# Performance work log

Measured on AMD Instinct MI355X. Metric: run time of the kernel, lower is better.

## Reference

```python
import jax, jax.numpy as jnp
import numpy as np

T, H, E, K, I = 8192, 1024, 8, 2, 512  # tokens, hidden, experts, top_k, expert_intermediate
IS = I * 1  # shared-expert intermediate = expert_intermediate_size * num_shared_experts


def setup_inputs() -> dict:
    key = jax.random.key(0)
    ks = jax.random.split(key, 6)
    s = lambda *d: 1.0 / np.sqrt(d[0])
    return {
        "hidden_states": jax.random.normal(ks[0], (T, H), dtype=jnp.float32),
        "w_gate": jax.random.normal(ks[1], (H, E), dtype=jnp.float32) * s(H),
        "w_experts_gate_up": jax.random.normal(ks[2], (E, H, 2 * I), dtype=jnp.float32) * s(H),
        "w_experts_down": jax.random.normal(ks[3], (E, I, H), dtype=jnp.float32) * s(I),
        "w_shared_gate_up": jax.random.normal(ks[4], (H, 2 * IS), dtype=jnp.float32) * s(H),
        "w_shared_down": jax.random.normal(ks[5], (IS, H), dtype=jnp.float32) * s(IS),
    }


def _silu_and_mul(gu):
    d = gu.shape[-1] // 2
    return jax.nn.silu(gu[..., :d]) * gu[..., d:]


def reference(hidden_states, w_gate, w_experts_gate_up, w_experts_down,
              w_shared_gate_up, w_shared_down):
    x = hidden_states  # [T, H]

    # shared expert: SwiGLU MLP (reduce_results=False path)
    shared_out = _silu_and_mul(x @ w_shared_gate_up) @ w_shared_down  # [T, H]

    # router gate + top-k with renormalization (norm_expert_prob=True)
    router_logits = x @ w_gate  # [T, E]
    probs = jax.nn.softmax(router_logits.astype(jnp.float32), axis=-1)
    topk_w, topk_idx = jax.lax.top_k(probs, K)  # [T, K]
    topk_w = topk_w / jnp.sum(topk_w, axis=-1, keepdims=True)
    # scatter top-k weights into a sparse [T, E] combine matrix
    full_w = jnp.zeros((T, E), dtype=x.dtype)
    full_w = full_w.at[jnp.arange(T)[:, None], topk_idx].set(topk_w.astype(x.dtype))

    # expert SwiGLU MLPs (grouped GEMM expressed as batched einsum over experts)
    gu = jnp.einsum('th,ehi->eti', x, w_experts_gate_up)       # [E, T, 2I]
    act = _silu_and_mul(gu)                                     # [E, T, I]
    expert_out = jnp.einsum('eti,eih->eth', act, w_experts_down)  # [E, T, H]

    # weighted combine over selected experts (weights are zero elsewhere)
    moe_out = jnp.einsum('te,eth->th', full_w, expert_out)     # [T, H]

    return moe_out + shared_out
```

## Files before the change

### kernel.cpp

```cpp
#include <hip/hip_runtime.h>
#include <hip/hip_bf16.h>
#include <cstdint>

#define T_TOK 8192
#define HID   1024
#define NE    9
#define ISZ   512
#define RBASE 18432
#define NSLOT (RBASE + T_TOK)

#define BM 256
#define NROWB (NSLOT / BM)

typedef unsigned short u16;
typedef unsigned int   u32;
typedef signed char    i8;
typedef __attribute__((ext_vector_type(8))) short short8;
typedef __attribute__((ext_vector_type(4))) float f32x4;
typedef __attribute__((ext_vector_type(4))) int   i32x4;

__device__ __forceinline__ u16 f2bf(float f) {
  u32 u = __builtin_bit_cast(u32, f);
  return (u16)((u + 0x7fffu + ((u >> 16) & 1u)) >> 16);
}
__device__ __forceinline__ float bf2f(u16 v) {
  return __builtin_bit_cast(float, (u32)v << 16);
}
__device__ __forceinline__ int q8(float v, float inv) {
  int q = (int)__builtin_rintf(v * inv);
  return (q > 127) ? 127 : ((q < -127) ? -127 : q);
}

#define STAGE(gp, lp) __builtin_amdgcn_global_load_lds( \
    (__attribute__((address_space(1))) u32*)(gp),       \
    (__attribute__((address_space(3))) u32*)(lp), 16, 0, 0)

__global__ void k_zero(int* wam) { if (threadIdx.x < 16) wam[threadIdx.x] = 0; }

__global__ __launch_bounds__(256) void k_wamax(
    const float* __restrict__ wgu, const float* __restrict__ wsg, int* __restrict__ wam) {
  const int e = blockIdx.y;
  const float* src = (e < 8) ? (wgu + (size_t)e * 1048576) : wsg;
  float m = 0.f;
  for (int i = blockIdx.x * 256 + threadIdx.x; i < 262144; i += 16 * 256) {
    float4 v = ((const float4*)src)[i];
    m = fmaxf(m, fmaxf(fmaxf(fabsf(v.x), fabsf(v.y)), fmaxf(fabsf(v.z), fabsf(v.w))));
  }
#pragma unroll
  for (int off = 32; off >= 1; off >>= 1) m = fmaxf(m, __shfl_xor(m, off));
  __shared__ float sm[4];
  if ((threadIdx.x & 63) == 0) sm[threadIdx.x >> 6] = m;
  __syncthreads();
  if (threadIdx.x == 0) {
    m = fmaxf(fmaxf(sm[0], sm[1]), fmaxf(sm[2], sm[3]));
    atomicMax(wam + e, __float_as_int(m));
  }
}

#define NB_WGUP (32 * 32 * NE)
#define NB_WDN  (32 * 16 * NE)
#define NB_RTR  (T_TOK / 4)

__global__ __launch_bounds__(256) void k_prep(
    const float* __restrict__ x, const float* __restrict__ wg,
    const float* __restrict__ wgu, const float* __restrict__ wsg,
    const float* __restrict__ wdn, const float* __restrict__ wsd,
    const int* __restrict__ wam,
    i8* __restrict__ xq, float* __restrict__ sxg,
    i8* __restrict__ wguq, u16* __restrict__ wdT,
    int* __restrict__ eidx, float2* __restrict__ wts) {
  __shared__ float tile[32][33];
  const int b = blockIdx.x;
  const int tid = threadIdx.x;

  if (b < NB_WGUP) {
    const int e = b / 1024, rem = b % 1024;
    const int c0 = (rem & 31) * 32, h0 = (rem >> 5) * 32;
    const float* src = (e < 8) ? (wgu + (size_t)e * HID * 1024) : wsg;
    const float invw = 127.f / __int_as_float(wam[e]);
    const int tx = tid & 31, ty = tid >> 5;
    for (int i = ty; i < 32; i += 8)
      tile[i][tx] = src[(size_t)(h0 + i) * 1024 + c0 + tx];
    __syncthreads();
    for (int j = ty; j < 32; j += 8) {
      int c = c0 + j;
      int i = (c < 512) ? c : (c - 512);
      int colp = ((i >> 4) * 32) + ((c < 512) ? 0 : 16) + (i & 15);
      wguq[((size_t)e * 1024 + colp) * HID + h0 + tx] = (i8)q8(tile[tx][j], invw);
    }
    return;
  }
  if (b < NB_WGUP + NB_WDN) {
    const int bb = b - NB_WGUP;
    const int e = bb / 512, rem = bb % 512;
    const int h0 = (rem & 31) * 32, i0 = (rem >> 5) * 32;
    const float* src = (e < 8) ? (wdn + (size_t)e * ISZ * HID) : wsd;
    const int tx = tid & 31, ty = tid >> 5;
    for (int a = ty; a < 32; a += 8)
      tile[a][tx] = src[(size_t)(i0 + a) * HID + h0 + tx];
    __syncthreads();
    for (int j = ty; j < 32; j += 8)
      wdT[((size_t)e * HID + h0 + j) * ISZ + i0 + tx] = f2bf(tile[tx][j]);
    return;
  }
  const int t = (b - NB_WGUP - NB_WDN) * 4 + (tid >> 6);
  const int l = tid & 63;
  float a[8] = {0, 0, 0, 0, 0, 0, 0, 0};
  float vals[16];
  float am = 0.f;
  const float4* xr4 = (const float4*)(x + (size_t)t * HID);
#pragma unroll
  for (int j = 0; j < 4; ++j) {
    const float4 v = xr4[j * 64 + l];
    vals[4 * j] = v.x; vals[4 * j + 1] = v.y; vals[4 * j + 2] = v.z; vals[4 * j + 3] = v.w;
    am = fmaxf(am, fmaxf(fmaxf(fabsf(v.x), fabsf(v.y)), fmaxf(fabsf(v.z), fabsf(v.w))));
    const int h = (j * 64 + l) * 4;
#pragma unroll
    for (int i = 0; i < 4; ++i) {
      const float4 w0 = *(const float4*)&wg[(h + i) * 8];
      const float4 w1 = *(const float4*)&wg[(h + i) * 8 + 4];
      const float ev = vals[4 * j + i];
      a[0] += ev * w0.x; a[1] += ev * w0.y; a[2] += ev * w0.z; a[3] += ev * w0.w;
      a[4] += ev * w1.x; a[5] += ev * w1.y; a[6] += ev * w1.z; a[7] += ev * w1.w;
    }
  }
#pragma unroll
  for (int off = 32; off >= 1; off >>= 1) {
    am = fmaxf(am, __shfl_xor(am, off));
#pragma unroll
    for (int e2 = 0; e2 < 8; ++e2) a[e2] += __shfl_xor(a[e2], off);
  }
  const float inv = (am > 0.f) ? 127.f / am : 0.f;
  u32* xq4 = (u32*)(xq + (size_t)t * HID);
#pragma unroll
  for (int j = 0; j < 4; ++j) {
    u32 q = ((u32)(unsigned char)(i8)q8(vals[4 * j], inv)) |
            ((u32)(unsigned char)(i8)q8(vals[4 * j + 1], inv) << 8) |
            ((u32)(unsigned char)(i8)q8(vals[4 * j + 2], inv) << 16) |
            ((u32)(unsigned char)(i8)q8(vals[4 * j + 3], inv) << 24);
    xq4[j * 64 + l] = q;
  }
  if (l == 0) {
    sxg[t] = am * (1.f / 127.f);
    int ia = 0;
#pragma unroll
    for (int e2 = 1; e2 < 8; ++e2) if (a[e2] > a[ia]) ia = e2;
    int ib = (ia == 0) ? 1 : 0;
#pragma unroll
    for (int e2 = 0; e2 < 8; ++e2) if (e2 != ia && a[e2] > a[ib]) ib = e2;
    float wa = 1.f / (1.f + expf(a[ib] - a[ia]));
    eidx[t] = ia | (ib << 8);
    wts[t] = make_float2(wa, 1.f - wa);
  }
}

__global__ __launch_bounds__(512) void k_scatter(
    const int* __restrict__ eidx, int* __restrict__ btok, int* __restrict__ slotmap,
    int* __restrict__ seg, int* __restrict__ segcnt) {
  __shared__ int cnt_s[8];
  __shared__ int goff_s[9];
  const int e = threadIdx.x >> 6;
  const int l = threadIdx.x & 63;

  int c1 = 0;
  for (int c = 0; c < T_TOK / 64; ++c) {
    int v = eidx[c * 64 + l];
    c1 += __popcll(__ballot((v & 255) == e)) + __popcll(__ballot(((v >> 8) & 255) == e));
  }
  if (l == 0) cnt_s[e] = c1;
  __syncthreads();
  if (threadIdx.x == 0) {
    int off = 0;
    for (int k = 0; k < 8; ++k) { goff_s[k] = off; off += (cnt_s[k] + 255) & ~255; }
    goff_s[8] = off;
  }
  __syncthreads();
  const int base0 = goff_s[e];
  const int cnt_e = cnt_s[e];
  const unsigned long long below = (l == 63) ? ~0ull >> 1 : ((1ull << l) - 1);

  int base = base0;
  for (int c = 0; c < T_TOK / 64; ++c) {
    const int t = c * 64 + l;
    const int v = eidx[t];
    const unsigned long long ma = __ballot((v & 255) == e);
    const unsigned long long mb = __ballot(((v >> 8) & 255) == e);
    if ((v & 255) == e) {
      int s = base + __popcll(ma & below);
      btok[s] = t; slotmap[2 * t] = s;
    }
    if (((v >> 8) & 255) == e) {
      int s = base + __popcll(ma) + __popcll(mb & below);
      btok[s] = t; slotmap[2 * t + 1] = s;
    }
    base += __popcll(ma) + __popcll(mb);
  }
  for (int p = cnt_e + l; p < ((cnt_e + 255) & ~255); p += 64) btok[base0 + p] = 0;
  if (threadIdx.x < 9) seg[threadIdx.x] = goff_s[threadIdx.x];
  if (threadIdx.x < 8) segcnt[threadIdx.x] = cnt_s[threadIdx.x];
}

__device__ __forceinline__ bool seg_lookup(const int* __restrict__ seg,
                                           const int* __restrict__ segcnt,
                                           int brow, int& e) {
  if (brow >= RBASE) { e = 8; return true; }
  if (brow >= seg[8]) return false;
  e = 0;
#pragma unroll
  for (int k = 1; k < 8; ++k) if (brow >= seg[k]) e = k;
  return brow < seg[e] + segcnt[e];
}


#define G1_STG(kt) do {                                             \
    const int _ra = ((kt) % 3) * 32768;                             \
    STAGE(sA0 + (kt) * 128, Ab + _ra + 0 * 8192 + w * 1024);        \
    STAGE(sA1 + (kt) * 128, Ab + _ra + 1 * 8192 + w * 1024);        \
    STAGE(sA2 + (kt) * 128, Ab + _ra + 2 * 8192 + w * 1024);        \
    STAGE(sA3 + (kt) * 128, Ab + _ra + 3 * 8192 + w * 1024);        \
    const int _rb = ((kt) % 3) * 16384;                             \
    STAGE(sB0 + (kt) * 128, Bb + _rb + 0 * 8192 + w * 1024);        \
    STAGE(sB1 + (kt) * 128, Bb + _rb + 1 * 8192 + w * 1024); } while (0)

#define G1_LOADF(SA, SB, RG, KX) do {                               \
    _Pragma("unroll") for (int m = 0; m < 4; ++m)                   \
      SA[m] = *(const i32x4*)&Ab[(RG) * 32768 + aBase + m * 2048 + (KX)]; \
    _Pragma("unroll") for (int n = 0; n < 4; ++n)                   \
      SB[n] = *(const i32x4*)&Bb[(RG) * 16384 + bBase + n * 2048 + (KX)]; } while (0)

#define G1_MFMA(SA, SB) do { __builtin_amdgcn_s_setprio(1);         \
    _Pragma("unroll") for (int m = 0; m < 4; ++m)                   \
      _Pragma("unroll") for (int n = 0; n < 4; ++n)                 \
        acc[m][n] = __builtin_amdgcn_mfma_i32_16x16x64_i8(SA[m], SB[n], acc[m][n], 0, 0, 0); \
    __builtin_amdgcn_s_setprio(0); } while (0)

__global__ __launch_bounds__(512) void k_gemm_gu(
    const i8* __restrict__ xq,
    const i8* __restrict__ wguq,
    const int* __restrict__ seg, const int* __restrict__ segcnt,
    const int* __restrict__ btok, const float* __restrict__ sxg,
    const int* __restrict__ wam,
    u16* __restrict__ act)
{
  const int bid = blockIdx.x;
  const int brow = (bid % NROWB) * BM;
  const int bcol = (bid / NROWB) * 128;
  int e;
  if (!seg_lookup(seg, segcnt, brow, e)) return;

  __shared__ __align__(16) i8 Ab[3 * 32768];
  __shared__ __align__(16) i8 Bb[3 * 16384];
  __shared__ float sxl[BM];

  const int tid = threadIdx.x;
  const int w = tid >> 6, l = tid & 63;
  const int wm = w >> 1, wn = w & 1;
  const int fr = l & 15, fg = l >> 4;

  if (tid < BM) {
    const int rrow = brow + tid;
    const int tk = (e < 8) ? btok[rrow] : (rrow - RBASE);
    sxl[tid] = sxg[tk];
  }

  const int rr = w * 8 + (l >> 3);
  const int sw = ((l & 7) ^ (l >> 3)) * 16;
  int tr[4];
#pragma unroll
  for (int j = 0; j < 4; ++j) {
    const int gr = brow + j * 64 + rr;
    tr[j] = (e < 8) ? btok[gr] : (gr - RBASE);
  }
  const i8* sA0 = xq + (size_t)tr[0] * HID + sw;
  const i8* sA1 = xq + (size_t)tr[1] * HID + sw;
  const i8* sA2 = xq + (size_t)tr[2] * HID + sw;
  const i8* sA3 = xq + (size_t)tr[3] * HID + sw;
  const i8* sB0 = wguq + ((size_t)e * 1024 + bcol + 0 * 64 + rr) * HID + sw;
  const i8* sB1 = wguq + ((size_t)e * 1024 + bcol + 1 * 64 + rr) * HID + sw;

  const int aBase = (wm * 64 + fr) * 128;
  const int bBase = (wn * 64 + fr) * 128;
  const int kx0 = (fg ^ (fr & 7)) * 16;
  const int kx1 = kx0 ^ 64;

  i32x4 acc[4][4];
#pragma unroll
  for (int m = 0; m < 4; ++m)
#pragma unroll
    for (int n = 0; n < 4; ++n) acc[m][n] = (i32x4){0, 0, 0, 0};
  i32x4 fA0[4], fB0[4], fA1[4], fB1[4];

  const int NKT = HID / 128;
  G1_STG(0); G1_STG(1);
  asm volatile("s_waitcnt vmcnt(6)" ::: "memory");
  __builtin_amdgcn_s_barrier();
  for (int s = 0; s < NKT; ++s) {
    const int rg = s % 3;
    if (s + 2 < NKT) G1_STG(s + 2);
    G1_LOADF(fA0, fB0, rg, kx0);
    __builtin_amdgcn_sched_barrier(0);
    G1_LOADF(fA1, fB1, rg, kx1);
    asm volatile("s_waitcnt lgkmcnt(8)" ::: "memory");
    __builtin_amdgcn_sched_barrier(0);
    G1_MFMA(fA0, fB0);
    asm volatile("s_waitcnt lgkmcnt(0)" ::: "memory");
    __builtin_amdgcn_sched_barrier(0);
    G1_MFMA(fA1, fB1);
    if (s + 1 < NKT) {
      if (s + 2 < NKT) { asm volatile("s_waitcnt vmcnt(6)" ::: "memory"); }
      else             { asm volatile("s_waitcnt vmcnt(0)" ::: "memory"); }
      __builtin_amdgcn_s_barrier();
    }
  }

  const float swe = __int_as_float(wam[e]) * (1.f / 127.f);
#pragma unroll
  for (int m = 0; m < 4; ++m) {
#pragma unroll
    for (int p = 0; p < 2; ++p) {
      const i32x4 gI = acc[m][2 * p], uI = acc[m][2 * p + 1];
      const int col = ((bcol + wn * 64) >> 1) + p * 16 + fr;
#pragma unroll
      for (int r = 0; r < 4; ++r) {
        const int row_l = wm * 64 + m * 16 + fg * 4 + r;
        const float sc = sxl[row_l] * swe;
        const float gate = (float)gI[r] * sc;
        const float up   = (float)uI[r] * sc;
        const float sv = gate / (1.f + __expf(-gate));
        act[(size_t)(brow + row_l) * ISZ + col] = f2bf(sv * up);
      }
    }
  }
}


#define D_STGA(kt) do { const int _d = ((kt) % 3) * 8192 + w * 1024; \
    STAGE(dA0 + (kt) * 32, As + _d);                                 \
    STAGE(dA1 + (kt) * 32, As + _d + 512); } while (0)
#define D_STGB(kt) do { const int _d = ((kt) % 3) * 8192 + w * 1024; \
    STAGE(dB0 + (kt) * 32, Bs + _d);                                 \
    STAGE(dB1 + (kt) * 32, Bs + _d + 512); } while (0)
#define D_LDA4(sl, mb) do {                                          \
    af[0] = *(const short8*)&As[(sl) + aOff + ((mb) + 0) * 512];     \
    af[1] = *(const short8*)&As[(sl) + aOff + ((mb) + 1) * 512];     \
    af[2] = *(const short8*)&As[(sl) + aOff + ((mb) + 2) * 512];     \
    af[3] = *(const short8*)&As[(sl) + aOff + ((mb) + 3) * 512]; } while (0)
#define D_LDB4(sl) do {                                              \
    bf[0] = *(const short8*)&Bs[(sl) + bOff + 0 * 512];              \
    bf[1] = *(const short8*)&Bs[(sl) + bOff + 1 * 512];              \
    bf[2] = *(const short8*)&Bs[(sl) + bOff + 2 * 512];              \
    bf[3] = *(const short8*)&Bs[(sl) + bOff + 3 * 512]; } while (0)
#define D_MFMA16(mb) do { __builtin_amdgcn_s_setprio(1);             \
    _Pragma("unroll") for (int mm = 0; mm < 4; ++mm)                 \
      _Pragma("unroll") for (int nn = 0; nn < 4; ++nn)               \
        accf[(mb) + mm][nn] = __builtin_amdgcn_mfma_f32_16x16x32_bf16( \
            af[mm], bf[nn], accf[(mb) + mm][nn], 0, 0, 0);           \
    __builtin_amdgcn_s_setprio(0); } while (0)

__global__ __launch_bounds__(512) void k_gemm_down(
    const u16* __restrict__ act, const u16* __restrict__ wdT,
    const int* __restrict__ seg, const int* __restrict__ segcnt,
    u16* __restrict__ tmp) {
  const int brow = blockIdx.x * BM;
  const int bcol = blockIdx.y * 256;
  int e;
  if (!seg_lookup(seg, segcnt, brow, e)) return;

  __shared__ __align__(16) u16 As[3 * 8192];
  __shared__ __align__(16) u16 Bs[3 * 8192];

  const int tid = threadIdx.x;
  const int w = tid >> 6, l = tid & 63;
  const int wm = w >> 2, wn = w & 3;
  const int fr = l & 15, fg = l >> 4;

  const int arow0 = (w * 128 + l) >> 2;
  const int swd = ((l & 3) ^ (arow0 & 3)) * 8;
  const u16* dA0 = act + (size_t)(brow + arow0) * ISZ + swd;
  const u16* dA1 = act + (size_t)(brow + arow0 + 16) * ISZ + swd;
  const u16* dB0 = wdT + ((size_t)e * 1024 + bcol + arow0) * ISZ + swd;
  const u16* dB1 = wdT + ((size_t)e * 1024 + bcol + arow0 + 16) * ISZ + swd;

  const int aOff = (wm * 128 + fr) * 32 + ((fg ^ (fr & 3)) * 8);
  const int bOff = (wn * 64 + fr) * 32 + ((fg ^ (fr & 3)) * 8);

  f32x4 accf[8][4];
#pragma unroll
  for (int m = 0; m < 8; ++m)
#pragma unroll
    for (int n = 0; n < 4; ++n) accf[m][n] = (f32x4){0.f, 0.f, 0.f, 0.f};
  short8 af[4], bf[4];

  const int NKT = ISZ / 32;
  D_STGA(0); D_STGB(0); D_STGA(1); D_STGB(1);
  asm volatile("s_waitcnt vmcnt(4)" ::: "memory");
  __builtin_amdgcn_s_barrier();
  for (int kt = 0; kt < NKT; ++kt) {
    const int sl = (kt % 3) * 8192;
    D_LDA4(sl, 0); D_LDB4(sl);
    if (kt + 2 < NKT) D_STGA(kt + 2);
    __builtin_amdgcn_s_barrier();
    asm volatile("s_waitcnt lgkmcnt(0)" ::: "memory");
    __builtin_amdgcn_sched_barrier(0);
    D_MFMA16(0);
    __builtin_amdgcn_s_barrier();
    D_LDA4(sl, 4);
    if (kt + 2 < NKT) D_STGB(kt + 2);
    __builtin_amdgcn_s_barrier();
    asm volatile("s_waitcnt lgkmcnt(0)" ::: "memory");
    __builtin_amdgcn_sched_barrier(0);
    D_MFMA16(4);
    if (kt + 2 < NKT)      { asm volatile("s_waitcnt vmcnt(4)" ::: "memory"); }
    else if (kt + 1 < NKT) { asm volatile("s_waitcnt vmcnt(0)" ::: "memory"); }
    __builtin_amdgcn_s_barrier();
  }

#pragma unroll
  for (int m = 0; m < 8; ++m) {
#pragma unroll
    for (int r = 0; r < 4; ++r) {
      const int row = brow + wm * 128 + m * 16 + fg * 4 + r;
#pragma unroll
      for (int n = 0; n < 4; ++n) {
        const int col = bcol + wn * 64 + n * 16 + fr;
        tmp[(size_t)row * HID + col] = f2bf(accf[m][n][r]);
      }
    }
  }
}

__global__ __launch_bounds__(256) void k_combine(
    const u16* __restrict__ tmp, const int* __restrict__ slotmap,
    const float2* __restrict__ wts, float* __restrict__ out) {
  const int idx = blockIdx.x * 256 + threadIdx.x;
  const int t = idx >> 7;
  const int c = (idx & 127) << 3;
  const int s0 = slotmap[2 * t], s1 = slotmap[2 * t + 1];
  const float2 wv = wts[t];
  const short8 a = *(const short8*)(tmp + (size_t)s0 * HID + c);
  const short8 b = *(const short8*)(tmp + (size_t)s1 * HID + c);
  const short8 s = *(const short8*)(tmp + (size_t)(RBASE + t) * HID + c);
  float r[8];
#pragma unroll
  for (int j = 0; j < 8; ++j)
    r[j] = bf2f((u16)s[j]) + wv.x * bf2f((u16)a[j]) + wv.y * bf2f((u16)b[j]);
  float* po = out + (size_t)t * HID + c;
  *(float4*)po       = make_float4(r[0], r[1], r[2], r[3]);
  *(float4*)(po + 4) = make_float4(r[4], r[5], r[6], r[7]);
}

extern "C" void kernel_launch(void* const* d_in, const int* in_sizes, int n_in,
                              void* d_out, int out_size, void* d_ws, size_t ws_size,
                              hipStream_t stream) {
  const float* x   = (const float*)d_in[0];
  const float* wg  = (const float*)d_in[1];
  const float* wgu = (const float*)d_in[2];
  const float* wdn = (const float*)d_in[3];
  const float* wsg = (const float*)d_in[4];
  const float* wsd = (const float*)d_in[5];
  float* out = (float*)d_out;

  char* ws = (char*)d_ws;
  i8*  xq    = (i8*)ws;   ws += (size_t)T_TOK * HID;
  i8*  wguq  = (i8*)ws;   ws += (size_t)NE * 1024 * HID;
  u16* wdT   = (u16*)ws;  ws += (size_t)NE * HID * ISZ * 2;
  u16* actb  = (u16*)ws;  ws += (size_t)NSLOT * ISZ * 2;
  u16* tmp   = (u16*)ws;  ws += (size_t)NSLOT * HID * 2;
  float* sxg = (float*)ws; ws += (size_t)T_TOK * 4;
  int* eidx  = (int*)ws;  ws += (size_t)T_TOK * 4;
  float2* wt = (float2*)ws; ws += (size_t)T_TOK * 8;
  int* btok  = (int*)ws;  ws += (size_t)RBASE * 4;
  int* smap  = (int*)ws;  ws += (size_t)2 * T_TOK * 4;
  int* seg   = (int*)ws;  ws += 16 * 4;
  int* segc  = (int*)ws;  ws += 16 * 4;
  int* wam   = (int*)ws;

  k_zero<<<1, 64, 0, stream>>>(wam);
  k_wamax<<<dim3(16, NE), 256, 0, stream>>>(wgu, wsg, wam);
  k_prep<<<NB_WGUP + NB_WDN + NB_RTR, 256, 0, stream>>>(
      x, wg, wgu, wsg, wdn, wsd, wam, xq, sxg, wguq, wdT, eidx, wt);
  k_scatter<<<1, 512, 0, stream>>>(eidx, btok, smap, seg, segc);
  k_gemm_gu<<<NROWB * 8, 512, 0, stream>>>(
      xq, wguq, seg, segc, btok, sxg, wam, actb);
  k_gemm_down<<<dim3(NROWB, HID / 256), 512, 0, stream>>>(actb, wdT, seg, segc, tmp);
  k_combine<<<(T_TOK * HID / 8) / 256, 256, 0, stream>>>(tmp, smap, wt, out);
}
```

Measured before the change: 213.5 us.

## Use per-column int8 weight scales and vectorize weight prep transposes

Replaces the per-expert max-abs weight scale with a per-output-column scale computed by a new column-reduction kernel, which removes the zero kernel and the atomics. The gate/up GEMM epilogue now reads per-column scales from shared memory. The weight quantize and transpose blocks in the prep kernel now cover larger tiles with float4 loads and 16-byte stores, cutting block count and store transactions. The per-column scales change numerics (likely more accurate), and the column max kernel reads with a strided, column-oriented pattern.

```diff
diff --git a/kernel.cpp b/kernel.cpp
--- a/kernel.cpp
+++ b/kernel.cpp
@@ -30,77 +30,97 @@
   int q = (int)__builtin_rintf(v * inv);
   return (q > 127) ? 127 : ((q < -127) ? -127 : q);
 }
+__device__ __forceinline__ int colp_of(int c) {
+  int i = (c < 512) ? c : (c - 512);
+  return (i >> 4) * 32 + ((c < 512) ? 0 : 16) + (i & 15);
+}
 
 #define STAGE(gp, lp) __builtin_amdgcn_global_load_lds( \
     (__attribute__((address_space(1))) u32*)(gp),       \
     (__attribute__((address_space(3))) u32*)(lp), 16, 0, 0)
 
-__global__ void k_zero(int* wam) { if (threadIdx.x < 16) wam[threadIdx.x] = 0; }
-
-__global__ __launch_bounds__(256) void k_wamax(
-    const float* __restrict__ wgu, const float* __restrict__ wsg, int* __restrict__ wam) {
+__global__ __launch_bounds__(256) void k_wamax_col(
+    const float* __restrict__ wgu, const float* __restrict__ wsg,
+    float* __restrict__ swc) {
   const int e = blockIdx.y;
   const float* src = (e < 8) ? (wgu + (size_t)e * 1048576) : wsg;
+  const int c = blockIdx.x * 64 + (threadIdx.x & 63);
+  const int hs = threadIdx.x >> 6;
   float m = 0.f;
-  for (int i = blockIdx.x * 256 + threadIdx.x; i < 262144; i += 16 * 256) {
-    float4 v = ((const float4*)src)[i];
-    m = fmaxf(m, fmaxf(fmaxf(fabsf(v.x), fabsf(v.y)), fmaxf(fabsf(v.z), fabsf(v.w))));
-  }
-#pragma unroll
-  for (int off = 32; off >= 1; off >>= 1) m = fmaxf(m, __shfl_xor(m, off));
-  __shared__ float sm[4];
-  if ((threadIdx.x & 63) == 0) sm[threadIdx.x >> 6] = m;
+  for (int h = hs; h < HID; h += 4)
+    m = fmaxf(m, fabsf(src[(size_t)h * 1024 + c]));
+  __shared__ float red[4][64];
+  red[hs][threadIdx.x & 63] = m;
   __syncthreads();
-  if (threadIdx.x == 0) {
-    m = fmaxf(fmaxf(sm[0], sm[1]), fmaxf(sm[2], sm[3]));
-    atomicMax(wam + e, __float_as_int(m));
-  }
-}
-
-#define NB_WGUP (32 * 32 * NE)
-#define NB_WDN  (32 * 16 * NE)
+  if (threadIdx.x < 64) {
+    const int cc = blockIdx.x * 64 + threadIdx.x;
+    m = fmaxf(fmaxf(red[0][threadIdx.x], red[1][threadIdx.x]),
+              fmaxf(red[2][threadIdx.x], red[3][threadIdx.x]));
+    swc[e * 1024 + colp_of(cc)] = m * (1.f / 127.f);
+  }
+}
+
+#define NB_WGUP (32 * 8 * NE)
+#define NB_WDN  (32 * 4 * NE)
 #define NB_RTR  (T_TOK / 4)
 
 __global__ __launch_bounds__(256) void k_prep(
     const float* __restrict__ x, const float* __restrict__ wg,
     const float* __restrict__ wgu, const float* __restrict__ wsg,
     const float* __restrict__ wdn, const float* __restrict__ wsd,
-    const int* __restrict__ wam,
+    const float* __restrict__ swc,
     i8* __restrict__ xq, float* __restrict__ sxg,
     i8* __restrict__ wguq, u16* __restrict__ wdT,
     int* __restrict__ eidx, float2* __restrict__ wts) {
-  __shared__ float tile[32][33];
+  __shared__ float tile[32][129];
   const int b = blockIdx.x;
   const int tid = threadIdx.x;
 
   if (b < NB_WGUP) {
-    const int e = b / 1024, rem = b % 1024;
-    const int c0 = (rem & 31) * 32, h0 = (rem >> 5) * 32;
+    const int e = b / 256, rem = b % 256;
+    const int c0 = (rem & 31) * 32, h0 = (rem >> 5) * 128;
     const float* src = (e < 8) ? (wgu + (size_t)e * HID * 1024) : wsg;
-    const float invw = 127.f / __int_as_float(wam[e]);
-    const int tx = tid & 31, ty = tid >> 5;
-    for (int i = ty; i < 32; i += 8)
-      tile[i][tx] = src[(size_t)(h0 + i) * 1024 + c0 + tx];
+    const int hl = tid >> 1, cb = (tid & 1) * 16;
+#pragma unroll
+    for (int j = 0; j < 4; ++j) {
+      const float4 v = *(const float4*)&src[(size_t)(h0 + hl) * 1024 + c0 + cb + j * 4];
+      tile[cb + j * 4 + 0][hl] = v.x;
+      tile[cb + j * 4 + 1][hl] = v.y;
+      tile[cb + j * 4 + 2][hl] = v.z;
+      tile[cb + j * 4 + 3][hl] = v.w;
+    }
     __syncthreads();
-    for (int j = ty; j < 32; j += 8) {
-      int c = c0 + j;
-      int i = (c < 512) ? c : (c - 512);
-      int colp = ((i >> 4) * 32) + ((c < 512) ? 0 : 16) + (i & 15);
-      wguq[((size_t)e * 1024 + colp) * HID + h0 + tx] = (i8)q8(tile[tx][j], invw);
-    }
+    const int cl = tid >> 3, hb = (tid & 7) * 16;
+    const int cp = colp_of(c0 + cl);
+    const float inv = 1.f / swc[e * 1024 + cp];
+    i8 out[16];
+#pragma unroll
+    for (int k = 0; k < 16; ++k) out[k] = (i8)q8(tile[cl][hb + k], inv);
+    *(int4*)&wguq[((size_t)e * 1024 + cp) * 1024 + h0 + hb] = *(int4*)out;
     return;
   }
   if (b < NB_WGUP + NB_WDN) {
     const int bb = b - NB_WGUP;
-    const int e = bb / 512, rem = bb % 512;
-    const int h0 = (rem & 31) * 32, i0 = (rem >> 5) * 32;
+    const int e = bb / 128, r2 = bb % 128;
+    const int h0 = (r2 & 31) * 32, i0 = (r2 >> 5) * 128;
     const float* src = (e < 8) ? (wdn + (size_t)e * ISZ * HID) : wsd;
-    const int tx = tid & 31, ty = tid >> 5;
-    for (int a = ty; a < 32; a += 8)
-      tile[a][tx] = src[(size_t)(i0 + a) * HID + h0 + tx];
+    const int il = tid >> 1, hb2 = (tid & 1) * 16;
+#pragma unroll
+    for (int j = 0; j < 4; ++j) {
+      const float4 v = *(const float4*)&src[(size_t)(i0 + il) * 1024 + h0 + hb2 + j * 4];
+      tile[hb2 + j * 4 + 0][il] = v.x;
+      tile[hb2 + j * 4 + 1][il] = v.y;
+      tile[hb2 + j * 4 + 2][il] = v.z;
+      tile[hb2 + j * 4 + 3][il] = v.w;
+    }
     __syncthreads();
-    for (int j = ty; j < 32; j += 8)
-      wdT[((size_t)e * HID + h0 + j) * ISZ + i0 + tx] = f2bf(tile[tx][j]);
+    const int hl2 = tid >> 3, ib = (tid & 7) * 16;
+    u16 ob[16];
+#pragma unroll
+    for (int k = 0; k < 16; ++k) ob[k] = f2bf(tile[hl2][ib + k]);
+    u16* dst = &wdT[((size_t)e * HID + h0 + hl2) * ISZ + i0 + ib];
+    *(int4*)dst = *(int4*)ob;
+    *(int4*)(dst + 8) = *(int4*)(ob + 8);
     return;
   }
   const int t = (b - NB_WGUP - NB_WDN) * 4 + (tid >> 6);
@@ -239,7 +259,7 @@
     const i8* __restrict__ wguq,
     const int* __restrict__ seg, const int* __restrict__ segcnt,
     const int* __restrict__ btok, const float* __restrict__ sxg,
-    const int* __restrict__ wam,
+    const float* __restrict__ swc,
     u16* __restrict__ act)
 {
   const int bid = blockIdx.x;
@@ -251,6 +271,7 @@
   __shared__ __align__(16) i8 Ab[3 * 32768];
   __shared__ __align__(16) i8 Bb[3 * 16384];
   __shared__ float sxl[BM];
+  __shared__ float swcl[128];
 
   const int tid = threadIdx.x;
   const int w = tid >> 6, l = tid & 63;
@@ -262,6 +283,7 @@
     const int tk = (e < 8) ? btok[rrow] : (rrow - RBASE);
     sxl[tid] = sxg[tk];
   }
+  if (tid >= BM && tid < BM + 128) swcl[tid - BM] = swc[e * 1024 + bcol + (tid - BM)];
 
   const int rr = w * 8 + (l >> 3);
   const int sw = ((l & 7) ^ (l >> 3)) * 16;
@@ -313,19 +335,20 @@
     }
   }
 
-  const float swe = __int_as_float(wam[e]) * (1.f / 127.f);
 #pragma unroll
   for (int m = 0; m < 4; ++m) {
 #pragma unroll
     for (int p = 0; p < 2; ++p) {
       const i32x4 gI = acc[m][2 * p], uI = acc[m][2 * p + 1];
       const int col = ((bcol + wn * 64) >> 1) + p * 16 + fr;
+      const float swg = swcl[wn * 64 + p * 32 + fr];
+      const float swu = swcl[wn * 64 + p * 32 + 16 + fr];
 #pragma unroll
       for (int r = 0; r < 4; ++r) {
         const int row_l = wm * 64 + m * 16 + fg * 4 + r;
-        const float sc = sxl[row_l] * swe;
-        const float gate = (float)gI[r] * sc;
-        const float up   = (float)uI[r] * sc;
+        const float sx = sxl[row_l];
+        const float gate = (float)gI[r] * (sx * swg);
+        const float up   = (float)uI[r] * (sx * swu);
         const float sv = gate / (1.f + __expf(-gate));
         act[(size_t)(brow + row_l) * ISZ + col] = f2bf(sv * up);
       }
@@ -467,21 +490,20 @@
   u16* actb  = (u16*)ws;  ws += (size_t)NSLOT * ISZ * 2;
   u16* tmp   = (u16*)ws;  ws += (size_t)NSLOT * HID * 2;
   float* sxg = (float*)ws; ws += (size_t)T_TOK * 4;
+  float* swc = (float*)ws; ws += (size_t)NE * 1024 * 4;
   int* eidx  = (int*)ws;  ws += (size_t)T_TOK * 4;
   float2* wt = (float2*)ws; ws += (size_t)T_TOK * 8;
   int* btok  = (int*)ws;  ws += (size_t)RBASE * 4;
   int* smap  = (int*)ws;  ws += (size_t)2 * T_TOK * 4;
   int* seg   = (int*)ws;  ws += 16 * 4;
-  int* segc  = (int*)ws;  ws += 16 * 4;
-  int* wam   = (int*)ws;
-
-  k_zero<<<1, 64, 0, stream>>>(wam);
-  k_wamax<<<dim3(16, NE), 256, 0, stream>>>(wgu, wsg, wam);
+  int* segc  = (int*)ws;
+
+  k_wamax_col<<<dim3(16, NE), 256, 0, stream>>>(wgu, wsg, swc);
   k_prep<<<NB_WGUP + NB_WDN + NB_RTR, 256, 0, stream>>>(
-      x, wg, wgu, wsg, wdn, wsd, wam, xq, sxg, wguq, wdT, eidx, wt);
+      x, wg, wgu, wsg, wdn, wsd, swc, xq, sxg, wguq, wdT, eidx, wt);
   k_scatter<<<1, 512, 0, stream>>>(eidx, btok, smap, seg, segc);
   k_gemm_gu<<<NROWB * 8, 512, 0, stream>>>(
-      xq, wguq, seg, segc, btok, sxg, wam, actb);
+      xq, wguq, seg, segc, btok, sxg, swc, actb);
   k_gemm_down<<<dim3(NROWB, HID / 256), 512, 0, stream>>>(actb, wdT, seg, segc, tmp);
   k_combine<<<(T_TOK * HID / 8) / 256, 256, 0, stream>>>(tmp, smap, wt, out);
 }
```

New measurement: 239.2 us. 1.12x slower.
